# Kernel optimization log

Measured on AMD Instinct MI355X. Metric: run time of the kernel, lower is better.

## Reference

```python
import jax, jax.numpy as jnp
import numpy as np

B, N, D, H = 128, 32768, 768, 16
DH = D // H          # per-head hidden_size = memory_dim // num_heads = 48
BETA = 0.25          # scaling (inverse temperature)
STEPS = 5            # update_steps_max
TOPK = 4


def _ln(x, g, b):
    # torch nn.LayerNorm over last dim (biased variance, eps=1e-5), affine
    m = jnp.mean(x, axis=-1, keepdims=True)
    v = jnp.var(x, axis=-1, keepdims=True)
    return (x - m) * jax.lax.rsqrt(v + 1e-5) * g + b


def _l2norm(x):
    # F.normalize(x, dim=-1): x / max(||x||, 1e-12)
    n = jnp.linalg.norm(x, axis=-1, keepdims=True)
    return x / jnp.maximum(n, 1e-12)


def setup_inputs() -> dict:
    key = jax.random.key(0)
    ks = jax.random.split(key, 8)
    s = 0.05  # weight init scale to keep activations sane
    return {
        "query_embedding": jax.random.normal(ks[0], (B, D), jnp.float32),
        "memory_bank": jax.random.normal(ks[1], (N, D), jnp.float32),
        "ln_k_g": jnp.ones((D,), jnp.float32), "ln_k_b": jnp.zeros((D,), jnp.float32),
        "ln_q_g": jnp.ones((D,), jnp.float32), "ln_q_b": jnp.zeros((D,), jnp.float32),
        "ln_v_g": jnp.ones((D,), jnp.float32), "ln_v_b": jnp.zeros((D,), jnp.float32),
        "Wq": jax.random.normal(ks[2], (D, D), jnp.float32) * s, "bq": jnp.zeros((D,), jnp.float32),
        "Wk": jax.random.normal(ks[3], (D, D), jnp.float32) * s, "bk": jnp.zeros((D,), jnp.float32),
        "Wv": jax.random.normal(ks[4], (D, D), jnp.float32) * s, "bv": jnp.zeros((D,), jnp.float32),
        "Wo": jax.random.normal(ks[5], (D, D), jnp.float32) * s, "bo": jnp.zeros((D,), jnp.float32),
        "W1": jax.random.normal(ks[6], (D, D), jnp.float32) * s, "b1": jnp.zeros((D,), jnp.float32),
        "W2": jax.random.normal(ks[7], (D, D), jnp.float32) * s, "b2": jnp.zeros((D,), jnp.float32),
    }


def reference(query_embedding, memory_bank, ln_k_g, ln_k_b, ln_q_g, ln_q_b,
              ln_v_g, ln_v_b, Wq, bq, Wk, bk, Wv, bv, Wo, bo, W1, b1, W2, b2):
    # Affine LayerNorms on stored pattern, state pattern, pattern projection.
    # memory_bank is shared across the batch, so normalize/project it ONCE
    # instead of materializing the (B, N, D) expand from the torch code.
    stored = _ln(memory_bank, ln_k_g, ln_k_b)        # (N, D)
    state = _ln(query_embedding, ln_q_g, ln_q_b)     # (B, D) -- state pattern, seq len 1
    projp = _ln(memory_bank, ln_v_g, ln_v_b)         # (N, D)

    k = (stored @ Wk.T + bk).reshape(N, H, DH)       # (N, H, dh)
    v = (projp @ Wv.T + bv).reshape(N, H, DH)        # (N, H, dh)
    q = (state @ Wq.T + bq).reshape(B, H, DH)        # (B, H, dh)

    # Hopfield convergence: xi <- softmax(beta * xi K^T) K, repeated STEPS times
    def step(xi, _):
        attn = jax.nn.softmax(BETA * jnp.einsum('bhd,nhd->bhn', xi, k), axis=-1)
        return jnp.einsum('bhn,nhd->bhd', attn, k), None

    xi, _ = jax.lax.scan(step, q, None, length=STEPS)

    # Final readout against the (separately normalized) pattern projection V
    attn = jax.nn.softmax(BETA * jnp.einsum('bhd,nhd->bhn', xi, k), axis=-1)  # (B, H, N)
    converged = jnp.einsum('bhn,nhd->bhd', attn, v).reshape(B, D) @ Wo.T + bo  # (B, D)

    # Retrieval head: residual + MLP + cosine-sim logits + top-k
    combined = query_embedding + converged
    rq = jax.nn.relu(combined @ W1.T + b1) @ W2.T + b2
    logits = (_l2norm(rq) @ _l2norm(memory_bank).T) * 20.0   # (B, N)
    top_indices = jax.lax.top_k(logits, TOPK)[1]              # (B, TOPK)
    return top_indices, logits
```

## Files before the change

### kernel.cpp

```cpp
#include <hip/hip_runtime.h>
#include <math.h>

#define NTOT 32768
#define DMODEL 768
#define BSZ 128
#define NHEAD 16
#define DH 48
#define BETA 0.25f

typedef _Float16 f16;
typedef f16 f16x8 __attribute__((ext_vector_type(8)));
typedef f16 f16x4 __attribute__((ext_vector_type(4)));
typedef float f32x4 __attribute__((ext_vector_type(4)));

__global__ __launch_bounds__(256)
void row_stats(const float* __restrict__ X, int M, float* __restrict__ mean,
               float* __restrict__ rstd, float* __restrict__ l2inv) {
  const int row = blockIdx.x * 4 + (threadIdx.x >> 6);
  const int lane = threadIdx.x & 63;
  if (row >= M) return;
  const float* x = X + (size_t)row * DMODEL;
  float s = 0.f, s2 = 0.f;
  for (int i = lane; i < DMODEL; i += 64) {
    float v = x[i];
    s += v; s2 += v * v;
  }
#pragma unroll
  for (int off = 32; off; off >>= 1) {
    s  += __shfl_xor(s, off);
    s2 += __shfl_xor(s2, off);
  }
  if (lane == 0) {
    float mu = s * (1.f / DMODEL);
    float var = s2 * (1.f / DMODEL) - mu * mu;
    mean[row] = mu;
    rstd[row] = rsqrtf(var + 1e-5f);
    if (l2inv) l2inv[row] = 1.f / fmaxf(sqrtf(s2), 1e-12f);
  }
}

__global__ __launch_bounds__(256)
void stats_norm_mb(const float* __restrict__ mb, f16* __restrict__ nh_hi,
                   f16* __restrict__ nh_lo, float* __restrict__ c1,
                   float* __restrict__ c2) {
  const int row = blockIdx.x * 4 + (threadIdx.x >> 6);
  const int lane = threadIdx.x & 63;
  const float* x = mb + (size_t)row * DMODEL;
  float v[12];
  float s = 0.f, s2 = 0.f;
#pragma unroll
  for (int j = 0; j < 3; j++) {
    const float4 v4 = *(const float4*)(x + lane * 4 + j * 256);
    v[j * 4 + 0] = v4.x; v[j * 4 + 1] = v4.y;
    v[j * 4 + 2] = v4.z; v[j * 4 + 3] = v4.w;
    s += v4.x + v4.y + v4.z + v4.w;
    s2 += v4.x * v4.x + v4.y * v4.y + v4.z * v4.z + v4.w * v4.w;
  }
#pragma unroll
  for (int off = 32; off; off >>= 1) {
    s  += __shfl_xor(s, off);
    s2 += __shfl_xor(s2, off);
  }
  const float mu = s * (1.f / DMODEL);
  const float var = s2 * (1.f / DMODEL) - mu * mu;
  const float istd = sqrtf(var + 1e-5f);
  const float rs = 1.f / istd;
  f16* oh = nh_hi + (size_t)row * DMODEL;
  f16* ol = nh_lo + (size_t)row * DMODEL;
#pragma unroll
  for (int j = 0; j < 3; j++) {
    f16x4 h4, l4;
#pragma unroll
    for (int q = 0; q < 4; q++) {
      const float sv = (v[j * 4 + q] - mu) * rs;
      const f16 h = (f16)sv;
      h4[q] = h;
      l4[q] = (f16)(sv - (float)h);
    }
    *(f16x4*)(oh + lane * 4 + j * 256) = h4;
    *(f16x4*)(ol + lane * 4 + j * 256) = l4;
  }
  if (lane == 0) {
    const float l2i = 1.f / fmaxf(sqrtf(s2), 1e-12f);
    c1[row] = 20.f * l2i * istd;
    c2[row] = 20.f * l2i * mu;
  }
}

__global__ __launch_bounds__(256)
void rq_prep(const float* __restrict__ rq, f16* __restrict__ hi,
             f16* __restrict__ lo, float* __restrict__ ainv,
             float* __restrict__ rqsum) {
  const int row = blockIdx.x * 4 + (threadIdx.x >> 6);
  const int lane = threadIdx.x & 63;
  const float* x = rq + (size_t)row * DMODEL;
  f16* oh = hi + (size_t)row * DMODEL;
  f16* ol = lo + (size_t)row * DMODEL;
  float s = 0.f, s2 = 0.f;
#pragma unroll
  for (int j = 0; j < 3; j++) {
    const int d = lane * 4 + j * 256;
    const float4 v4 = *(const float4*)(x + d);
    const float vv[4] = {v4.x, v4.y, v4.z, v4.w};
    f16x4 h4, l4;
#pragma unroll
    for (int q = 0; q < 4; q++) {
      s += vv[q]; s2 += vv[q] * vv[q];
      const f16 h = (f16)vv[q];
      h4[q] = h;
      l4[q] = (f16)(vv[q] - (float)h);
    }
    *(f16x4*)(oh + d) = h4;
    *(f16x4*)(ol + d) = l4;
  }
#pragma unroll
  for (int off = 32; off; off >>= 1) {
    s  += __shfl_xor(s, off);
    s2 += __shfl_xor(s2, off);
  }
  if (lane == 0) {
    rqsum[row] = s;
    ainv[row] = 1.f / fmaxf(sqrtf(s2), 1e-12f);
  }
}

__global__ __launch_bounds__(256)
void prep_w(const float* __restrict__ Wk, const float* __restrict__ bk,
            const float* __restrict__ gk, const float* __restrict__ blnk,
            const float* __restrict__ Wv, const float* __restrict__ bv,
            const float* __restrict__ gv, const float* __restrict__ blnv,
            f16* __restrict__ Wc_hi, f16* __restrict__ Wc_lo,
            float* __restrict__ biasc) {
  const int o = blockIdx.x * 4 + (threadIdx.x >> 6);
  const int lane = threadIdx.x & 63;
  const bool isK = o < DMODEL;
  const float* W = isK ? (Wk + (size_t)o * DMODEL)
                       : (Wv + (size_t)(o - DMODEL) * DMODEL);
  const float* g   = isK ? gk : gv;
  const float* bln = isK ? blnk : blnv;
  float bacc = 0.f;
  for (int d = lane * 4; d < DMODEL; d += 256) {
    const float4 wv = *(const float4*)(W + d);
    const float4 g4 = *(const float4*)(g + d);
    const float4 b4 = *(const float4*)(bln + d);
    bacc += wv.x * b4.x + wv.y * b4.y + wv.z * b4.z + wv.w * b4.w;
    const float sv[4] = {wv.x * g4.x * 16.f, wv.y * g4.y * 16.f,
                         wv.z * g4.z * 16.f, wv.w * g4.w * 16.f};
    f16x4 h4, l4;
#pragma unroll
    for (int j = 0; j < 4; j++) {
      const f16 h = (f16)sv[j];
      h4[j] = h;
      l4[j] = (f16)(sv[j] - (float)h);
    }
    *(f16x4*)(Wc_hi + (size_t)o * DMODEL + d) = h4;
    *(f16x4*)(Wc_lo + (size_t)o * DMODEL + d) = l4;
  }
#pragma unroll
  for (int off = 32; off; off >>= 1) bacc += __shfl_xor(bacc, off);
  if (lane == 0) biasc[o] = (isK ? bk[o] : bv[o - DMODEL]) + bacc;
}

__global__ __launch_bounds__(256)
void proj_dual_mfma(const f16* __restrict__ nh_hi, const f16* __restrict__ nh_lo,
                    const f16* __restrict__ Wc_hi, const f16* __restrict__ Wc_lo,
                    const float* __restrict__ biasc,
                    f16* __restrict__ k_hi, f16* __restrict__ k_lo,
                    f16* __restrict__ v_hi, f16* __restrict__ v_lo) {
  __shared__ __align__(16) f16 As[128][64];
  __shared__ __align__(16) f16 Bs[128][64];
  const int t = threadIdx.x;
  const int n0 = blockIdx.x * 128;
  const int m0 = blockIdx.y * 128;
  const int w = t >> 6, lane = t & 63;
  const int l15 = lane & 15, lq = lane >> 4;
  const int wm = w >> 1, wn = w & 1;
  const int sc = (lane & 7) ^ (lane >> 3);
  const int srow = lane >> 3;

  f32x4 acc[4][4];
#pragma unroll
  for (int a = 0; a < 4; a++)
#pragma unroll
    for (int b = 0; b < 4; b++)
#pragma unroll
      for (int r = 0; r < 4; r++) acc[a][b][r] = 0.f;

  for (int k0 = 0; k0 < DMODEL; k0 += 32) {
    __syncthreads();
#pragma unroll
    for (int i = 0; i < 4; i++) {
      const int rb = (w * 4 + i) * 8;
      const f16* asrc = ((sc < 4) ? nh_hi : nh_lo) +
          (size_t)(m0 + rb + srow) * DMODEL + k0 + (sc & 3) * 8;
      __builtin_amdgcn_global_load_lds(
          (__attribute__((address_space(1))) void*)asrc,
          (__attribute__((address_space(3))) void*)&As[rb][0], 16, 0, 0);
      const f16* bsrc = ((sc < 4) ? Wc_hi : Wc_lo) +
          (size_t)(n0 + rb + srow) * DMODEL + k0 + (sc & 3) * 8;
      __builtin_amdgcn_global_load_lds(
          (__attribute__((address_space(1))) void*)bsrc,
          (__attribute__((address_space(3))) void*)&Bs[rb][0], 16, 0, 0);
    }
    __syncthreads();

    f16x8 nhh[4], nhl[4];
#pragma unroll
    for (int fm = 0; fm < 4; fm++) {
      const int row = wm * 64 + fm * 16 + l15;
      const int e = row & 7;
      nhh[fm] = *(const f16x8*)&As[row][(lq ^ e) * 8];
      nhl[fm] = *(const f16x8*)&As[row][((lq + 4) ^ e) * 8];
    }
    f16x8 wh[4], wl[4];
#pragma unroll
    for (int fo = 0; fo < 4; fo++) {
      const int row = wn * 64 + fo * 16 + l15;
      const int e = row & 7;
      wh[fo] = *(const f16x8*)&Bs[row][(lq ^ e) * 8];
      wl[fo] = *(const f16x8*)&Bs[row][((lq + 4) ^ e) * 8];
    }
#pragma unroll
    for (int fo = 0; fo < 4; fo++)
#pragma unroll
      for (int fm = 0; fm < 4; fm++) {
        f32x4 a = acc[fo][fm];
        a = __builtin_amdgcn_mfma_f32_16x16x32_f16(wh[fo], nhh[fm], a, 0, 0, 0);
        a = __builtin_amdgcn_mfma_f32_16x16x32_f16(wh[fo], nhl[fm], a, 0, 0, 0);
        a = __builtin_amdgcn_mfma_f32_16x16x32_f16(wl[fo], nhh[fm], a, 0, 0, 0);
        acc[fo][fm] = a;
      }
  }
  const int oc = n0 + wn * 64;
  const bool isK = oc < DMODEL;
  f16* oh = isK ? k_hi : v_hi;
  f16* ol = isK ? k_lo : v_lo;
  const int obase = (isK ? oc : oc - DMODEL) + lq * 4;
#pragma unroll
  for (int fo = 0; fo < 4; fo++) {
    const float4 bb = *(const float4*)(biasc + oc + fo * 16 + lq * 4);
    const float bbv[4] = {bb.x, bb.y, bb.z, bb.w};
    const int o = obase + fo * 16;
#pragma unroll
    for (int fm = 0; fm < 4; fm++) {
      const size_t moff = (size_t)(m0 + wm * 64 + fm * 16 + l15) * DMODEL + o;
      f16x4 h4, l4;
#pragma unroll
      for (int r = 0; r < 4; r++) {
        const float v = acc[fo][fm][r] * 0.0625f + bbv[r];
        const f16 h = (f16)v;
        h4[r] = h;
        l4[r] = (f16)(v - (float)h);
      }
      *(f16x4*)(oh + moff) = h4;
      *(f16x4*)(ol + moff) = l4;
    }
  }
}

__global__ __launch_bounds__(256)
void logits_mfma(const f16* __restrict__ nh_hi, const f16* __restrict__ nh_lo,
                 const f16* __restrict__ rq_hi, const f16* __restrict__ rq_lo,
                 const float* __restrict__ c1, const float* __restrict__ c2,
                 const float* __restrict__ ainv, const float* __restrict__ rqsum,
                 float* __restrict__ out) {
  __shared__ __align__(16) f16 As[128][64];
  __shared__ __align__(16) f16 Bs[128][64];
  const int t = threadIdx.x;
  const int n0 = blockIdx.x * 128;
  const int w = t >> 6, lane = t & 63;
  const int l15 = lane & 15, lq = lane >> 4;
  const int wm = w >> 1, wn = w & 1;
  const int sc = (lane & 7) ^ (lane >> 3);
  const int srow = lane >> 3;

  f32x4 acc[4][4];
#pragma unroll
  for (int a = 0; a < 4; a++)
#pragma unroll
    for (int b = 0; b < 4; b++)
#pragma unroll
      for (int r = 0; r < 4; r++) acc[a][b][r] = 0.f;

  for (int k0 = 0; k0 < DMODEL; k0 += 32) {
    __syncthreads();
#pragma unroll
    for (int i = 0; i < 4; i++) {
      const int rb = (w * 4 + i) * 8;
      const f16* asrc = ((sc < 4) ? nh_hi : nh_lo) +
          (size_t)(n0 + rb + srow) * DMODEL + k0 + (sc & 3) * 8;
      __builtin_amdgcn_global_load_lds(
          (__attribute__((address_space(1))) void*)asrc,
          (__attribute__((address_space(3))) void*)&As[rb][0], 16, 0, 0);
      const f16* bsrc = ((sc < 4) ? rq_hi : rq_lo) +
          (size_t)(rb + srow) * DMODEL + k0 + (sc & 3) * 8;
      __builtin_amdgcn_global_load_lds(
          (__attribute__((address_space(1))) void*)bsrc,
          (__attribute__((address_space(3))) void*)&Bs[rb][0], 16, 0, 0);
    }
    __syncthreads();

    f16x8 ah[4], al[4];
#pragma unroll
    for (int fo = 0; fo < 4; fo++) {
      const int row = wn * 64 + fo * 16 + l15;
      const int e = row & 7;
      ah[fo] = *(const f16x8*)&As[row][(lq ^ e) * 8];
      al[fo] = *(const f16x8*)&As[row][((lq + 4) ^ e) * 8];
    }
    f16x8 bh[4], bl[4];
#pragma unroll
    for (int fm = 0; fm < 4; fm++) {
      const int row = wm * 64 + fm * 16 + l15;
      const int e = row & 7;
      bh[fm] = *(const f16x8*)&Bs[row][(lq ^ e) * 8];
      bl[fm] = *(const f16x8*)&Bs[row][((lq + 4) ^ e) * 8];
    }
#pragma unroll
    for (int fo = 0; fo < 4; fo++)
#pragma unroll
      for (int fm = 0; fm < 4; fm++) {
        f32x4 a = acc[fo][fm];
        a = __builtin_amdgcn_mfma_f32_16x16x32_f16(ah[fo], bh[fm], a, 0, 0, 0);
        a = __builtin_amdgcn_mfma_f32_16x16x32_f16(ah[fo], bl[fm], a, 0, 0, 0);
        a = __builtin_amdgcn_mfma_f32_16x16x32_f16(al[fo], bh[fm], a, 0, 0, 0);
        acc[fo][fm] = a;
      }
  }
#pragma unroll
  for (int fm = 0; fm < 4; fm++) {
    const int b = wm * 64 + fm * 16 + l15;
    const float am = ainv[b];
    const float rs = rqsum[b];
#pragma unroll
    for (int fo = 0; fo < 4; fo++) {
      const int nb = n0 + wn * 64 + fo * 16 + lq * 4;
      const float4 c1v = *(const float4*)(c1 + nb);
      const float4 c2v = *(const float4*)(c2 + nb);
      const float c1a[4] = {c1v.x, c1v.y, c1v.z, c1v.w};
      const float c2a[4] = {c2v.x, c2v.y, c2v.z, c2v.w};
      float4 o4;
      float ov[4];
#pragma unroll
      for (int r = 0; r < 4; r++)
        ov[r] = am * (acc[fo][fm][r] * c1a[r] + rs * c2a[r]);
      o4.x = ov[0]; o4.y = ov[1]; o4.z = ov[2]; o4.w = ov[3];
      *(float4*)(out + (size_t)b * NTOT + nb) = o4;
    }
  }
}

__global__ __launch_bounds__(256)
void ln_gemm_f32(const float* __restrict__ A, const float* __restrict__ mean,
                 const float* __restrict__ rstd, const float* __restrict__ g,
                 const float* __restrict__ bln, const float* __restrict__ W,
                 const float* __restrict__ bias, float* __restrict__ out) {
  __shared__ float As[16][68];
  __shared__ float Ws[16][68];
  const int t = threadIdx.x;
  const int m0 = blockIdx.y << 6, n0 = blockIdx.x << 6;
  const int tm = t >> 4, tn = t & 15;
  const int lr = t >> 2;
  const int lk = (t & 3) << 2;
  const float muL = mean[m0 + lr];
  const float rsL = rstd[m0 + lr];
  float acc[4][4] = {};
  for (int k0 = 0; k0 < DMODEL; k0 += 16) {
    float4 a4 = *(const float4*)(A + (size_t)(m0 + lr) * DMODEL + k0 + lk);
    float4 g4 = *(const float4*)(g + k0 + lk);
    float4 b4 = *(const float4*)(bln + k0 + lk);
    As[lk + 0][lr] = (a4.x - muL) * rsL * g4.x + b4.x;
    As[lk + 1][lr] = (a4.y - muL) * rsL * g4.y + b4.y;
    As[lk + 2][lr] = (a4.z - muL) * rsL * g4.z + b4.z;
    As[lk + 3][lr] = (a4.w - muL) * rsL * g4.w + b4.w;
    float4 w4 = *(const float4*)(W + (size_t)(n0 + lr) * DMODEL + k0 + lk);
    Ws[lk + 0][lr] = w4.x;
    Ws[lk + 1][lr] = w4.y;
    Ws[lk + 2][lr] = w4.z;
    Ws[lk + 3][lr] = w4.w;
    __syncthreads();
#pragma unroll
    for (int kk = 0; kk < 16; kk++) {
      const float4 av = *(const float4*)(&As[kk][tm * 4]);
      const float4 bv = *(const float4*)(&Ws[kk][tn * 4]);
      const float a[4] = {av.x, av.y, av.z, av.w};
      const float b[4] = {bv.x, bv.y, bv.z, bv.w};
#pragma unroll
      for (int i = 0; i < 4; i++)
#pragma unroll
        for (int j = 0; j < 4; j++) acc[i][j] += a[i] * b[j];
    }
    __syncthreads();
  }
  const float4 bia = *(const float4*)(bias + n0 + tn * 4);
  const float bb[4] = {bia.x, bia.y, bia.z, bia.w};
#pragma unroll
  for (int i = 0; i < 4; i++) {
    const int m = m0 + tm * 4 + i;
    float4 o4;
    o4.x = acc[i][0] + bb[0];
    o4.y = acc[i][1] + bb[1];
    o4.z = acc[i][2] + bb[2];
    o4.w = acc[i][3] + bb[3];
    *(float4*)(out + (size_t)m * DMODEL + n0 + tn * 4) = o4;
  }
}

__global__ __launch_bounds__(256)
void gemm_bias(const float* __restrict__ A, const float* __restrict__ W,
               const float* __restrict__ bias, const float* __restrict__ add,
               float* __restrict__ out, int relu) {
  __shared__ float As[16][68];
  __shared__ float Ws[16][68];
  const int t = threadIdx.x;
  const int m0 = blockIdx.y << 6, n0 = blockIdx.x << 6;
  const int tm = t >> 4, tn = t & 15;
  const int lr = t >> 2;
  const int lk = (t & 3) << 2;
  float acc[4][4] = {};
  for (int k0 = 0; k0 < DMODEL; k0 += 16) {
    float4 a4 = *(const float4*)(A + (size_t)(m0 + lr) * DMODEL + k0 + lk);
    As[lk + 0][lr] = a4.x;
    As[lk + 1][lr] = a4.y;
    As[lk + 2][lr] = a4.z;
    As[lk + 3][lr] = a4.w;
    float4 w4 = *(const float4*)(W + (size_t)(n0 + lr) * DMODEL + k0 + lk);
    Ws[lk + 0][lr] = w4.x;
    Ws[lk + 1][lr] = w4.y;
    Ws[lk + 2][lr] = w4.z;
    Ws[lk + 3][lr] = w4.w;
    __syncthreads();
#pragma unroll
    for (int kk = 0; kk < 16; kk++) {
      const float4 av = *(const float4*)(&As[kk][tm * 4]);
      const float4 bv = *(const float4*)(&Ws[kk][tn * 4]);
      const float a[4] = {av.x, av.y, av.z, av.w};
      const float b[4] = {bv.x, bv.y, bv.z, bv.w};
#pragma unroll
      for (int i = 0; i < 4; i++)
#pragma unroll
        for (int j = 0; j < 4; j++) acc[i][j] += a[i] * b[j];
    }
    __syncthreads();
  }
  const float4 bia = *(const float4*)(bias + n0 + tn * 4);
  const float bb[4] = {bia.x, bia.y, bia.z, bia.w};
#pragma unroll
  for (int i = 0; i < 4; i++) {
    const int m = m0 + tm * 4 + i;
    float v[4];
#pragma unroll
    for (int j = 0; j < 4; j++) v[j] = acc[i][j] + bb[j];
    if (add) {
      const float4 a4 = *(const float4*)(add + (size_t)m * DMODEL + n0 + tn * 4);
      v[0] += a4.x; v[1] += a4.y; v[2] += a4.z; v[3] += a4.w;
    }
    if (relu) {
#pragma unroll
      for (int j = 0; j < 4; j++) v[j] = fmaxf(v[j], 0.f);
    }
    float4 o4 = {v[0], v[1], v[2], v[3]};
    *(float4*)(out + (size_t)m * DMODEL + n0 + tn * 4) = o4;
  }
}

__global__ __launch_bounds__(256)
void split_xi_k(const float* __restrict__ xi, f16* __restrict__ hi,
                f16* __restrict__ lo) {
  const int i = blockIdx.x * 256 + threadIdx.x;
  float4 v = ((const float4*)xi)[i];
  float s[4] = {v.x * BETA, v.y * BETA, v.z * BETA, v.w * BETA};
  f16x4 h4, l4;
#pragma unroll
  for (int j = 0; j < 4; j++) {
    f16 h = (f16)s[j];
    h4[j] = h;
    l4[j] = (f16)(s[j] - (float)h);
  }
  ((f16x4*)hi)[i] = h4;
  ((f16x4*)lo)[i] = l4;
}

#define FCHUNK 64
#define FROWS (NTOT / FCHUNK)

__global__ __launch_bounds__(256)
void flash_round(const f16* __restrict__ k_hi, const f16* __restrict__ k_lo,
                 const f16* __restrict__ val_hi, const f16* __restrict__ val_lo,
                 const f16* __restrict__ xi_hi, const f16* __restrict__ xi_lo,
                 float* __restrict__ part_ml, float* __restrict__ part_o) {
  const int h = blockIdx.y, chunk = blockIdx.x;
  const int tid = threadIdx.x, w = tid >> 6, lane = tid & 63;
  const int l15 = lane & 15, lq = lane >> 4;
  const int b0 = w * 32;

  __shared__ __align__(16) f16 krow[2][32][56];
  __shared__ __align__(16) f16 vT[2][48][40];
  __shared__ __align__(16) f16 pHi[4][32][40];
  __shared__ __align__(16) f16 pLo[4][32][40];

  const f16x8 zf = {};
  f16x8 xqh[2][2], xql[2][2];
#pragma unroll
  for (int bt = 0; bt < 2; bt++) {
    const size_t xoff = (size_t)(b0 + bt * 16 + l15) * DMODEL + h * DH;
    xqh[bt][0] = *(const f16x8*)(xi_hi + xoff + lq * 8);
    xql[bt][0] = *(const f16x8*)(xi_lo + xoff + lq * 8);
    const size_t xo1 = xoff + 32 + (lq & 1) * 8;
    f16x8 th = *(const f16x8*)(xi_hi + xo1);
    f16x8 tl = *(const f16x8*)(xi_lo + xo1);
    xqh[bt][1] = (lq < 2) ? th : zf;
    xql[bt][1] = (lq < 2) ? tl : zf;
  }

  float m[2] = {-1e30f, -1e30f}, lsum[2] = {0.f, 0.f};
  f32x4 O[3][2];
#pragma unroll
  for (int mt = 0; mt < 3; mt++)
#pragma unroll
    for (int bt = 0; bt < 2; bt++)
#pragma unroll
      for (int j = 0; j < 4; j++) O[mt][bt][j] = 0.f;

  const int nbase = chunk * FROWS;
  for (int it = 0; it < FROWS / 32; it++) {
    const int gn0 = nbase + it * 32;
    __syncthreads();
    for (int j = tid; j < 384; j += 256) {
      const int tsel = j / 192;
      const int q = j - tsel * 192;
      const int r = q / 6;
      const int d0 = (q - r * 6) * 8;
      const size_t goff = (size_t)(gn0 + r) * DMODEL + h * DH + d0;
      const f16* kp = (tsel ? k_lo : k_hi) + goff;
      const f16* vp = (tsel ? val_lo : val_hi) + goff;
      f16x8 kv = *(const f16x8*)kp;
      f16x8 vv = *(const f16x8*)vp;
      *(f16x8*)&krow[tsel][r][d0] = kv;
#pragma unroll
      for (int jj = 0; jj < 8; jj++) vT[tsel][d0 + jj][r] = vv[jj];
    }
    __syncthreads();

    f16x8 akh[2][2], akl[2][2];
#pragma unroll
    for (int nt = 0; nt < 2; nt++) {
      const int row = nt * 16 + l15;
      akh[nt][0] = *(const f16x8*)&krow[0][row][lq * 8];
      akl[nt][0] = *(const f16x8*)&krow[1][row][lq * 8];
      f16x8 t0 = *(const f16x8*)&krow[0][row][32 + (lq & 1) * 8];
      f16x8 t1 = *(const f16x8*)&krow[1][row][32 + (lq & 1) * 8];
      akh[nt][1] = (lq < 2) ? t0 : zf;
      akl[nt][1] = (lq < 2) ? t1 : zf;
    }
    f32x4 S[2][2];
#pragma unroll
    for (int nt = 0; nt < 2; nt++)
#pragma unroll
      for (int bt = 0; bt < 2; bt++) {
        f32x4 s = {};
        s = __builtin_amdgcn_mfma_f32_16x16x32_f16(akh[nt][0], xqh[bt][0], s, 0, 0, 0);
        s = __builtin_amdgcn_mfma_f32_16x16x32_f16(akh[nt][1], xqh[bt][1], s, 0, 0, 0);
        s = __builtin_amdgcn_mfma_f32_16x16x32_f16(akh[nt][0], xql[bt][0], s, 0, 0, 0);
        s = __builtin_amdgcn_mfma_f32_16x16x32_f16(akh[nt][1], xql[bt][1], s, 0, 0, 0);
        s = __builtin_amdgcn_mfma_f32_16x16x32_f16(akl[nt][0], xqh[bt][0], s, 0, 0, 0);
        s = __builtin_amdgcn_mfma_f32_16x16x32_f16(akl[nt][1], xqh[bt][1], s, 0, 0, 0);
        S[nt][bt] = s;
      }
    float sc[2];
#pragma unroll
    for (int bt = 0; bt < 2; bt++) {
      float mx = S[0][bt][0];
#pragma unroll
      for (int r = 1; r < 4; r++) mx = fmaxf(mx, S[0][bt][r]);
#pragma unroll
      for (int r = 0; r < 4; r++) mx = fmaxf(mx, S[1][bt][r]);
      mx = fmaxf(mx, __shfl_xor(mx, 16));
      mx = fmaxf(mx, __shfl_xor(mx, 32));
      const float mnew = fmaxf(m[bt], mx);
      sc[bt] = __expf(m[bt] - mnew);
      float ps = 0.f;
#pragma unroll
      for (int nt = 0; nt < 2; nt++) {
        f16x4 ph, pl;
#pragma unroll
        for (int r = 0; r < 4; r++) {
          const float p = __expf(S[nt][bt][r] - mnew);
          ps += p;
          const f16 hh = (f16)p;
          ph[r] = hh;
          pl[r] = (f16)(p - (float)hh);
        }
        *(f16x4*)&pHi[w][bt * 16 + l15][nt * 16 + lq * 4] = ph;
        *(f16x4*)&pLo[w][bt * 16 + l15][nt * 16 + lq * 4] = pl;
      }
      ps += __shfl_xor(ps, 16);
      ps += __shfl_xor(ps, 32);
      lsum[bt] = lsum[bt] * sc[bt] + ps;
      m[bt] = mnew;
    }
    __asm__ volatile("s_waitcnt lgkmcnt(0)" ::: "memory");
    f16x8 avh[3], avl[3];
#pragma unroll
    for (int mt = 0; mt < 3; mt++) {
      avh[mt] = *(const f16x8*)&vT[0][mt * 16 + l15][lq * 8];
      avl[mt] = *(const f16x8*)&vT[1][mt * 16 + l15][lq * 8];
    }
    f16x8 pbh[2], pbl[2];
#pragma unroll
    for (int bt = 0; bt < 2; bt++) {
      pbh[bt] = *(const f16x8*)&pHi[w][bt * 16 + l15][lq * 8];
      pbl[bt] = *(const f16x8*)&pLo[w][bt * 16 + l15][lq * 8];
    }
#pragma unroll
    for (int mt = 0; mt < 3; mt++)
#pragma unroll
      for (int bt = 0; bt < 2; bt++) {
#pragma unroll
        for (int j = 0; j < 4; j++) O[mt][bt][j] *= sc[bt];
        f32x4 o = O[mt][bt];
        o = __builtin_amdgcn_mfma_f32_16x16x32_f16(avh[mt], pbh[bt], o, 0, 0, 0);
        o = __builtin_amdgcn_mfma_f32_16x16x32_f16(avh[mt], pbl[bt], o, 0, 0, 0);
        o = __builtin_amdgcn_mfma_f32_16x16x32_f16(avl[mt], pbh[bt], o, 0, 0, 0);
        O[mt][bt] = o;
      }
  }
  const int pc = h * FCHUNK + chunk;
  if (lq == 0) {
#pragma unroll
    for (int bt = 0; bt < 2; bt++) {
      float* pm = part_ml + ((size_t)pc * BSZ + b0 + bt * 16 + l15) * 2;
      pm[0] = m[bt];
      pm[1] = lsum[bt];
    }
  }
#pragma unroll
  for (int mt = 0; mt < 3; mt++)
#pragma unroll
    for (int bt = 0; bt < 2; bt++) {
      float* po = part_o + ((size_t)pc * BSZ + b0 + bt * 16 + l15) * 48 +
                  mt * 16 + lq * 4;
      *(f32x4*)po = O[mt][bt];
    }
}

__global__ __launch_bounds__(64)
void hopfield_combine(const float* __restrict__ part_ml,
                      const float* __restrict__ part_o, float* __restrict__ dst) {
  const int bh = blockIdx.x;
  const int h = bh >> 7, b = bh & 127;
  const int c = threadIdx.x;
  __shared__ float w[64];
  const float* pm = part_ml + ((size_t)(h * 64 + c) * BSZ + b) * 2;
  const float mp = pm[0];
  const float lp = pm[1];
  float M = mp;
#pragma unroll
  for (int off = 32; off; off >>= 1) M = fmaxf(M, __shfl_xor(M, off));
  const float wp = __expf(mp - M);
  w[c] = wp;
  float L = lp * wp;
#pragma unroll
  for (int off = 32; off; off >>= 1) L += __shfl_xor(L, off);
  __syncthreads();
  if (c < DH) {
    float o = 0.f;
    for (int p = 0; p < 64; p++)
      o += part_o[((size_t)(h * 64 + p) * BSZ + b) * 48 + c] * w[p];
    dst[(size_t)b * DMODEL + h * DH + c] = o / L;
  }
}

__global__ __launch_bounds__(256)
void topk_kernel(const float* __restrict__ logits, float* __restrict__ outIdx) {
  const int b = blockIdx.x;
  const int t = threadIdx.x;
  const float* row = logits + (size_t)b * NTOT;
  float v[4] = {-1e30f, -1e30f, -1e30f, -1e30f};
  int id[4] = {0x7fffffff, 0x7fffffff, 0x7fffffff, 0x7fffffff};
  for (int n = t; n < NTOT; n += 256) {
    const float x = row[n];
    if (x > v[3]) {
      v[3] = x; id[3] = n;
#pragma unroll
      for (int s = 3; s > 0; s--) {
        const bool sw = (v[s] > v[s - 1]) || (v[s] == v[s - 1] && id[s] < id[s - 1]);
        if (sw) {
          float tv = v[s]; v[s] = v[s - 1]; v[s - 1] = tv;
          int ti = id[s]; id[s] = id[s - 1]; id[s - 1] = ti;
        }
      }
    }
  }
  __shared__ float sv[256][4];
  __shared__ int si[256][4];
#pragma unroll
  for (int j = 0; j < 4; j++) { sv[t][j] = v[j]; si[t][j] = id[j]; }
  for (int str = 128; str >= 1; str >>= 1) {
    __syncthreads();
    if (t < str) {
      float a[4], c[4];
      int ai[4], ci[4];
#pragma unroll
      for (int j = 0; j < 4; j++) {
        a[j] = sv[t][j]; ai[j] = si[t][j];
        c[j] = sv[t + str][j]; ci[j] = si[t + str][j];
      }
      float rv[4]; int ri[4];
      int p = 0, q = 0;
#pragma unroll
      for (int oo = 0; oo < 4; oo++) {
        const bool ta = (a[p] > c[q]) || (a[p] == c[q] && ai[p] < ci[q]);
        if (ta) { rv[oo] = a[p]; ri[oo] = ai[p]; p++; }
        else    { rv[oo] = c[q]; ri[oo] = ci[q]; q++; }
      }
#pragma unroll
      for (int j = 0; j < 4; j++) { sv[t][j] = rv[j]; si[t][j] = ri[j]; }
    }
  }
  if (t == 0) {
#pragma unroll
    for (int j = 0; j < 4; j++) outIdx[b * 4 + j] = (float)si[0][j];
  }
}

extern "C" void kernel_launch(void* const* d_in, const int* in_sizes, int n_in,
                              void* d_out, int out_size, void* d_ws, size_t ws_size,
                              hipStream_t stream) {
  const float* qe    = (const float*)d_in[0];
  const float* mb    = (const float*)d_in[1];
  const float* ln_kg = (const float*)d_in[2];
  const float* ln_kb = (const float*)d_in[3];
  const float* ln_qg = (const float*)d_in[4];
  const float* ln_qb = (const float*)d_in[5];
  const float* ln_vg = (const float*)d_in[6];
  const float* ln_vb = (const float*)d_in[7];
  const float* Wq = (const float*)d_in[8];
  const float* bq = (const float*)d_in[9];
  const float* Wk = (const float*)d_in[10];
  const float* bk = (const float*)d_in[11];
  const float* Wv = (const float*)d_in[12];
  const float* bv = (const float*)d_in[13];
  const float* Wo = (const float*)d_in[14];
  const float* bo = (const float*)d_in[15];
  const float* W1 = (const float*)d_in[16];
  const float* b1 = (const float*)d_in[17];
  const float* W2 = (const float*)d_in[18];
  const float* b2 = (const float*)d_in[19];

  float* out = (float*)d_out;
  float* logits = out + BSZ * 4;

  float* ws = (float*)d_ws;
  size_t off = 0;
  auto alloc = [&](size_t n) { float* p = ws + off; off += n; return p; };
  const size_t ND2 = (size_t)NTOT * DMODEL / 2;
  float* c1      = alloc(NTOT);
  float* c2      = alloc(NTOT);
  float* q_mean  = alloc(128);
  float* q_rstd  = alloc(128);
  float* rq_inv  = alloc(128);
  float* rq_sum  = alloc(128);
  float* pad_    = alloc(256);
  f16* k_hi = (f16*)alloc(ND2);
  f16* k_lo = (f16*)alloc(ND2);
  f16* v_hi = (f16*)alloc(ND2);
  f16* v_lo = (f16*)alloc(ND2);
  f16* nh_hi = (f16*)alloc(ND2);
  f16* nh_lo = (f16*)alloc(ND2);
  float* part_ml = alloc((size_t)NHEAD * FCHUNK * BSZ * 2);
  float* part_o  = alloc((size_t)NHEAD * FCHUNK * BSZ * 48);
  float* xi   = alloc((size_t)BSZ * DMODEL);
  float* conv = alloc((size_t)BSZ * DMODEL);
  float* comb = alloc((size_t)BSZ * DMODEL);
  float* h1   = alloc((size_t)BSZ * DMODEL);
  f16* xi_hi = (f16*)alloc((size_t)BSZ * DMODEL / 2);
  f16* xi_lo = (f16*)alloc((size_t)BSZ * DMODEL / 2);
  f16* rq_hi = (f16*)alloc((size_t)BSZ * DMODEL / 2);
  f16* rq_lo = (f16*)alloc((size_t)BSZ * DMODEL / 2);
  f16* Wc_hi = (f16*)alloc((size_t)2 * DMODEL * DMODEL / 2);
  f16* Wc_lo = (f16*)alloc((size_t)2 * DMODEL * DMODEL / 2);
  float* biasc = alloc(2 * DMODEL);
  (void)ws_size; (void)in_sizes; (void)n_in; (void)out_size; (void)pad_;

  row_stats<<<BSZ / 4, 256, 0, stream>>>(qe, BSZ, q_mean, q_rstd, nullptr);
  stats_norm_mb<<<NTOT / 4, 256, 0, stream>>>(mb, nh_hi, nh_lo, c1, c2);
  prep_w<<<2 * DMODEL / 4, 256, 0, stream>>>(Wk, bk, ln_kg, ln_kb,
                                             Wv, bv, ln_vg, ln_vb,
                                             Wc_hi, Wc_lo, biasc);

  proj_dual_mfma<<<dim3(2 * DMODEL / 128, NTOT / 128), 256, 0, stream>>>(
      nh_hi, nh_lo, Wc_hi, Wc_lo, biasc, k_hi, k_lo, v_hi, v_lo);
  ln_gemm_f32<<<dim3(DMODEL / 64, BSZ / 64), 256, 0, stream>>>(
      qe, q_mean, q_rstd, ln_qg, ln_qb, Wq, bq, xi);

  for (int r = 0; r < 6; r++) {
    const f16* valHi = (r == 5) ? v_hi : k_hi;
    const f16* valLo = (r == 5) ? v_lo : k_lo;
    float* dst = (r == 5) ? conv : xi;
    split_xi_k<<<96, 256, 0, stream>>>(xi, xi_hi, xi_lo);
    flash_round<<<dim3(FCHUNK, NHEAD), 256, 0, stream>>>(
        k_hi, k_lo, valHi, valLo, xi_hi, xi_lo, part_ml, part_o);
    hopfield_combine<<<BSZ * NHEAD, 64, 0, stream>>>(part_ml, part_o, dst);
  }

  gemm_bias<<<dim3(DMODEL / 64, BSZ / 64), 256, 0, stream>>>(conv, Wo, bo, qe, comb, 0);
  gemm_bias<<<dim3(DMODEL / 64, BSZ / 64), 256, 0, stream>>>(comb, W1, b1, nullptr, h1, 1);
  float* rq = conv;
  gemm_bias<<<dim3(DMODEL / 64, BSZ / 64), 256, 0, stream>>>(h1, W2, b2, nullptr, rq, 0);

  rq_prep<<<BSZ / 4, 256, 0, stream>>>(rq, rq_hi, rq_lo, rq_inv, rq_sum);
  logits_mfma<<<NTOT / 128, 256, 0, stream>>>(nh_hi, nh_lo, rq_hi, rq_lo,
                                              c1, c2, rq_inv, rq_sum, logits);

  topk_kernel<<<BSZ, 256, 0, stream>>>(logits, out);
}
```

Before: 1.374 ms.

## Store value projection transposed and register-prefetch tiles in flash rounds

The projection kernel now also writes a transposed (head-dim by N) copy of its output, so flash_round can load the value tile with vector loads instead of scattering eight scalar LDS writes per element. The V projection is deferred and computed into the same transposed buffer just before the final readout round, which drops the V row-major buffers. flash_round now prefetches the next 32-row K and value tile into registers while computing on the current one. The cost is strided scalar global stores for the transposed output in the projection epilogue, an extra kernel launch, and an additional barrier per iteration.

Result: faster. 1.309 ms (-4.8%).

```diff
diff --git a/kernel.cpp b/kernel.cpp
--- a/kernel.cpp
+++ b/kernel.cpp
@@ -162,15 +162,15 @@
 }
 
 __global__ __launch_bounds__(256)
-void proj_dual_mfma(const f16* __restrict__ nh_hi, const f16* __restrict__ nh_lo,
-                    const f16* __restrict__ Wc_hi, const f16* __restrict__ Wc_lo,
-                    const float* __restrict__ biasc,
-                    f16* __restrict__ k_hi, f16* __restrict__ k_lo,
-                    f16* __restrict__ v_hi, f16* __restrict__ v_lo) {
+void proj_mfma(const f16* __restrict__ nh_hi, const f16* __restrict__ nh_lo,
+               const f16* __restrict__ Wc_hi, const f16* __restrict__ Wc_lo,
+               const float* __restrict__ biasc,
+               f16* __restrict__ k_hi, f16* __restrict__ k_lo,
+               f16* __restrict__ T_hi, f16* __restrict__ T_lo, int oc0) {
   __shared__ __align__(16) f16 As[128][64];
   __shared__ __align__(16) f16 Bs[128][64];
   const int t = threadIdx.x;
-  const int n0 = blockIdx.x * 128;
+  const int n0 = oc0 + blockIdx.x * 128;
   const int m0 = blockIdx.y * 128;
   const int w = t >> 6, lane = t & 63;
   const int l15 = lane & 15, lq = lane >> 4;
@@ -232,10 +232,8 @@
       }
   }
   const int oc = n0 + wn * 64;
-  const bool isK = oc < DMODEL;
-  f16* oh = isK ? k_hi : v_hi;
-  f16* ol = isK ? k_lo : v_lo;
-  const int obase = (isK ? oc : oc - DMODEL) + lq * 4;
+  const int obase = (oc - oc0) + lq * 4;
+  const bool wantRow = (oc0 == 0);
 #pragma unroll
   for (int fo = 0; fo < 4; fo++) {
     const float4 bb = *(const float4*)(biasc + oc + fo * 16 + lq * 4);
@@ -243,7 +241,7 @@
     const int o = obase + fo * 16;
 #pragma unroll
     for (int fm = 0; fm < 4; fm++) {
-      const size_t moff = (size_t)(m0 + wm * 64 + fm * 16 + l15) * DMODEL + o;
+      const int mrow = m0 + wm * 64 + fm * 16 + l15;
       f16x4 h4, l4;
 #pragma unroll
       for (int r = 0; r < 4; r++) {
@@ -252,8 +250,16 @@
         h4[r] = h;
         l4[r] = (f16)(v - (float)h);
       }
-      *(f16x4*)(oh + moff) = h4;
-      *(f16x4*)(ol + moff) = l4;
+      if (wantRow) {
+        const size_t moff = (size_t)mrow * DMODEL + o;
+        *(f16x4*)(k_hi + moff) = h4;
+        *(f16x4*)(k_lo + moff) = l4;
+      }
+#pragma unroll
+      for (int r = 0; r < 4; r++) {
+        T_hi[(size_t)(o + r) * NTOT + mrow] = h4[r];
+        T_lo[(size_t)(o + r) * NTOT + mrow] = l4[r];
+      }
     }
   }
 }
@@ -486,7 +492,7 @@
 
 __global__ __launch_bounds__(256)
 void flash_round(const f16* __restrict__ k_hi, const f16* __restrict__ k_lo,
-                 const f16* __restrict__ val_hi, const f16* __restrict__ val_lo,
+                 const f16* __restrict__ pvT_hi, const f16* __restrict__ pvT_lo,
                  const f16* __restrict__ xi_hi, const f16* __restrict__ xi_lo,
                  float* __restrict__ part_ml, float* __restrict__ part_o) {
   const int h = blockIdx.y, chunk = blockIdx.x;
@@ -495,9 +501,33 @@
   const int b0 = w * 32;
 
   __shared__ __align__(16) f16 krow[2][32][56];
-  __shared__ __align__(16) f16 vT[2][48][40];
+  __shared__ __align__(16) f16 ptT[2][48][40];
   __shared__ __align__(16) f16 pHi[4][32][40];
   __shared__ __align__(16) f16 pLo[4][32][40];
+
+  const int nbase = chunk * FROWS;
+
+  const f16* ssrc[3];
+  f16* sdst[3];
+  int sstep[3];
+#pragma unroll
+  for (int cc = 0; cc < 3; cc++) {
+    const int idx = cc * 256 + tid;
+    if (idx < 384) {
+      const int tsel = idx / 192, q = idx % 192;
+      const int r = q / 6, c = q % 6;
+      ssrc[cc] = (tsel ? k_lo : k_hi) + (size_t)(nbase + r) * DMODEL + h * DH + c * 8;
+      sdst[cc] = &krow[tsel][r][c * 8];
+      sstep[cc] = 32 * DMODEL;
+    } else {
+      const int j = idx - 384;
+      const int tsel = j / 192, q = j % 192;
+      const int d = q / 4, c = q % 4;
+      ssrc[cc] = (tsel ? pvT_lo : pvT_hi) + (size_t)(h * DH + d) * NTOT + nbase + c * 8;
+      sdst[cc] = &ptT[tsel][d][c * 8];
+      sstep[cc] = 32;
+    }
+  }
 
   const f16x8 zf = {};
   f16x8 xqh[2][2], xql[2][2];
@@ -522,25 +552,24 @@
 #pragma unroll
       for (int j = 0; j < 4; j++) O[mt][bt][j] = 0.f;
 
-  const int nbase = chunk * FROWS;
-  for (int it = 0; it < FROWS / 32; it++) {
-    const int gn0 = nbase + it * 32;
-    __syncthreads();
-    for (int j = tid; j < 384; j += 256) {
-      const int tsel = j / 192;
-      const int q = j - tsel * 192;
-      const int r = q / 6;
-      const int d0 = (q - r * 6) * 8;
-      const size_t goff = (size_t)(gn0 + r) * DMODEL + h * DH + d0;
-      const f16* kp = (tsel ? k_lo : k_hi) + goff;
-      const f16* vp = (tsel ? val_lo : val_hi) + goff;
-      f16x8 kv = *(const f16x8*)kp;
-      f16x8 vv = *(const f16x8*)vp;
-      *(f16x8*)&krow[tsel][r][d0] = kv;
-#pragma unroll
-      for (int jj = 0; jj < 8; jj++) vT[tsel][d0 + jj][r] = vv[jj];
-    }
-    __syncthreads();
+  f16x8 stg[3];
+#pragma unroll
+  for (int cc = 0; cc < 3; cc++) {
+    stg[cc] = *(const f16x8*)ssrc[cc];
+    ssrc[cc] += sstep[cc];
+  }
+#pragma unroll
+  for (int cc = 0; cc < 3; cc++) *(f16x8*)sdst[cc] = stg[cc];
+  __syncthreads();
+
+  for (int it = 0; it < 16; it++) {
+    if (it < 15) {
+#pragma unroll
+      for (int cc = 0; cc < 3; cc++) {
+        stg[cc] = *(const f16x8*)ssrc[cc];
+        ssrc[cc] += sstep[cc];
+      }
+    }
 
     f16x8 akh[2][2], akl[2][2];
 #pragma unroll
@@ -603,8 +632,8 @@
     f16x8 avh[3], avl[3];
 #pragma unroll
     for (int mt = 0; mt < 3; mt++) {
-      avh[mt] = *(const f16x8*)&vT[0][mt * 16 + l15][lq * 8];
-      avl[mt] = *(const f16x8*)&vT[1][mt * 16 + l15][lq * 8];
+      avh[mt] = *(const f16x8*)&ptT[0][mt * 16 + l15][lq * 8];
+      avl[mt] = *(const f16x8*)&ptT[1][mt * 16 + l15][lq * 8];
     }
     f16x8 pbh[2], pbl[2];
 #pragma unroll
@@ -624,6 +653,13 @@
         o = __builtin_amdgcn_mfma_f32_16x16x32_f16(avl[mt], pbh[bt], o, 0, 0, 0);
         O[mt][bt] = o;
       }
+
+    if (it < 15) {
+      __syncthreads();
+#pragma unroll
+      for (int cc = 0; cc < 3; cc++) *(f16x8*)sdst[cc] = stg[cc];
+      __syncthreads();
+    }
   }
   const int pc = h * FCHUNK + chunk;
   if (lq == 0) {
@@ -762,10 +798,10 @@
   float* rq_inv  = alloc(128);
   float* rq_sum  = alloc(128);
   float* pad_    = alloc(256);
-  f16* k_hi = (f16*)alloc(ND2);
-  f16* k_lo = (f16*)alloc(ND2);
-  f16* v_hi = (f16*)alloc(ND2);
-  f16* v_lo = (f16*)alloc(ND2);
+  f16* k_hi  = (f16*)alloc(ND2);
+  f16* k_lo  = (f16*)alloc(ND2);
+  f16* T_hi  = (f16*)alloc(ND2);
+  f16* T_lo  = (f16*)alloc(ND2);
   f16* nh_hi = (f16*)alloc(ND2);
   f16* nh_lo = (f16*)alloc(ND2);
   float* part_ml = alloc((size_t)NHEAD * FCHUNK * BSZ * 2);
@@ -789,20 +825,25 @@
                                              Wv, bv, ln_vg, ln_vb,
                                              Wc_hi, Wc_lo, biasc);
 
-  proj_dual_mfma<<<dim3(2 * DMODEL / 128, NTOT / 128), 256, 0, stream>>>(
-      nh_hi, nh_lo, Wc_hi, Wc_lo, biasc, k_hi, k_lo, v_hi, v_lo);
+  proj_mfma<<<dim3(DMODEL / 128, NTOT / 128), 256, 0, stream>>>(
+      nh_hi, nh_lo, Wc_hi, Wc_lo, biasc, k_hi, k_lo, T_hi, T_lo, 0);
   ln_gemm_f32<<<dim3(DMODEL / 64, BSZ / 64), 256, 0, stream>>>(
       qe, q_mean, q_rstd, ln_qg, ln_qb, Wq, bq, xi);
 
-  for (int r = 0; r < 6; r++) {
-    const f16* valHi = (r == 5) ? v_hi : k_hi;
-    const f16* valLo = (r == 5) ? v_lo : k_lo;
-    float* dst = (r == 5) ? conv : xi;
+  for (int r = 0; r < 5; r++) {
     split_xi_k<<<96, 256, 0, stream>>>(xi, xi_hi, xi_lo);
     flash_round<<<dim3(FCHUNK, NHEAD), 256, 0, stream>>>(
-        k_hi, k_lo, valHi, valLo, xi_hi, xi_lo, part_ml, part_o);
-    hopfield_combine<<<BSZ * NHEAD, 64, 0, stream>>>(part_ml, part_o, dst);
-  }
+        k_hi, k_lo, T_hi, T_lo, xi_hi, xi_lo, part_ml, part_o);
+    hopfield_combine<<<BSZ * NHEAD, 64, 0, stream>>>(part_ml, part_o, xi);
+  }
+
+  proj_mfma<<<dim3(DMODEL / 128, NTOT / 128), 256, 0, stream>>>(
+      nh_hi, nh_lo, Wc_hi, Wc_lo, biasc, k_hi, k_lo, T_hi, T_lo, DMODEL);
+
+  split_xi_k<<<96, 256, 0, stream>>>(xi, xi_hi, xi_lo);
+  flash_round<<<dim3(FCHUNK, NHEAD), 256, 0, stream>>>(
+      k_hi, k_lo, T_hi, T_lo, xi_hi, xi_lo, part_ml, part_o);
+  hopfield_combine<<<BSZ * NHEAD, 64, 0, stream>>>(part_ml, part_o, conv);
 
   gemm_bias<<<dim3(DMODEL / 64, BSZ / 64), 256, 0, stream>>>(conv, Wo, bo, qe, comb, 0);
   gemm_bias<<<dim3(DMODEL / 64, BSZ / 64), 256, 0, stream>>>(comb, W1, b1, nullptr, h1, 1);
```
